# Kernel optimization log

Measured on AMD Instinct MI355X. Metric: run time of the kernel, lower is better.

The kernel has to match this reference:

```python
import jax, jax.numpy as jnp
import numpy as np

B, S, K, N = 4, 2048, 4096, 11008
GROUP_SIZE = 128
NUM_GROUPS = K // GROUP_SIZE  # 32


def setup_inputs() -> dict:
    key = jax.random.key(0)
    k1, k2, k3, k4, k5 = jax.random.split(key, 5)
    x = jax.random.normal(k1, (B, S, K), dtype=jnp.float32)
    # sensitivity-sorted column order is a permutation of [0, K)
    col_indices = jax.random.permutation(k2, K).astype(jnp.int32)
    # packed uint8 nibbles stored as int32 in [0, 256)
    w_packed = jax.random.randint(k3, (K // 2, N), 0, 256, dtype=jnp.int32)
    # per-group, per-output-column dequant scales (positive, small)
    scales = (jax.random.uniform(k4, (NUM_GROUPS, N), dtype=jnp.float32) + 0.05) * 0.01
    bias = jax.random.normal(k5, (N,), dtype=jnp.float32) * 0.01
    return {"x": x, "col_indices": col_indices, "w_packed": w_packed,
            "scales": scales, "bias": bias}


def _dequant_weight(w_packed, scales):
    # unpack int4 nibbles: low nibble -> even k, high nibble -> odd k
    low = (w_packed & 15) - 8          # [K//2, N]
    high = ((w_packed >> 4) & 15) - 8  # [K//2, N]
    w_int = jnp.stack([low, high], axis=1).reshape(K, N)  # interleaved [K, N]
    # per-group dequant: scale index = k // group_size
    w = w_int.astype(scales.dtype).reshape(NUM_GROUPS, GROUP_SIZE, N)
    w = w * scales[:, None, :]
    return w.reshape(K, N)


def reference(x, col_indices, w_packed, scales, bias):
    orig_shape = x.shape
    xm = x.reshape(-1, K)                     # [M, K]
    xg = jnp.take(xm, col_indices, axis=1)    # column-reorder gather [M, K]
    w = _dequant_weight(w_packed, scales)     # [K, N]
    out = jnp.einsum('mk,kn->mn', xg, w)      # fp32 accumulate
    out = out + bias
    return out.reshape(orig_shape[0], orig_shape[1], N)
```

## Files before the change

kernel.cpp:

```cpp
#include <hip/hip_runtime.h>
#include <hip/hip_bf16.h>
#include <stdint.h>

#define M_DIM 8192
#define K_DIM 4096
#define N_DIM 11008

typedef __attribute__((ext_vector_type(8))) short bf16x8;
typedef __attribute__((ext_vector_type(4))) float f32x4;
typedef __attribute__((ext_vector_type(16))) float f32x16;
typedef __attribute__((ext_vector_type(4))) unsigned int uint4v;

__device__ __forceinline__ unsigned short f2bf(float f) {
    __hip_bfloat16 h = __float2bfloat16(f);
    return __builtin_bit_cast(unsigned short, h);
}

__device__ __forceinline__ void gload_lds16(const unsigned short* g, unsigned short* l) {
    __builtin_amdgcn_global_load_lds(
        (const __attribute__((address_space(1))) void*)g,
        (__attribute__((address_space(3))) void*)l,
        16, 0, 0);
}

__device__ __forceinline__ unsigned lds_addr(const unsigned short* p) {
    return (unsigned)(uintptr_t)(const __attribute__((address_space(3))) unsigned short*)p;
}

#define DSRI(dst, a, OFF) asm volatile("ds_read_b128 %0, %1 offset:%2" \
    : "=v"(dst) : "v"(a), "n"(OFF) : "memory")

#define LGKM(N) do { \
    asm volatile("s_waitcnt lgkmcnt(" #N ")" ::: "memory"); \
    __builtin_amdgcn_sched_barrier(0); \
} while (0)
#define BAR() do { __builtin_amdgcn_s_barrier(); asm volatile("" ::: "memory"); } while (0)

__global__ void permute_x_kernel(const float* __restrict__ x,
                                 const int* __restrict__ ci,
                                 unsigned short* __restrict__ xg) {
    int idx = blockIdx.x * 256 + threadIdx.x;
    int64_t base = (int64_t)idx * 4;
    int m = (int)(base >> 12);
    int k = (int)(base & 4095);
    const float* xrow = x + ((int64_t)m << 12);
    int4 c4 = *reinterpret_cast<const int4*>(ci + k);
    ushort4 o;
    o.x = f2bf(xrow[c4.x]);
    o.y = f2bf(xrow[c4.y]);
    o.z = f2bf(xrow[c4.z]);
    o.w = f2bf(xrow[c4.w]);
    *reinterpret_cast<ushort4*>(xg + base) = o;
}

__global__ void dequant_w_kernel(const int* __restrict__ wp,
                                 const float* __restrict__ scales,
                                 unsigned short* __restrict__ wT) {
    __shared__ unsigned short tile[64][65];
    int n0 = blockIdx.x * 64;
    int k0 = blockIdx.y * 64;
    int g = k0 >> 7;
    int t = threadIdx.x;
    int col = t & 63;
    int r0 = t >> 6;
    float s = scales[(int64_t)g * N_DIM + n0 + col];
    int pr0 = k0 >> 1;
#pragma unroll
    for (int i = 0; i < 8; ++i) {
        int row = r0 + i * 4;
        int p = wp[(int64_t)(pr0 + row) * N_DIM + n0 + col];
        tile[2 * row][col]     = f2bf((float)((p & 15) - 8) * s);
        tile[2 * row + 1][col] = f2bf((float)(((p >> 4) & 15) - 8) * s);
    }
    __syncthreads();
    int nl = t >> 2;
    int kk0 = (t & 3) << 4;
    unsigned short vals[16];
#pragma unroll
    for (int j = 0; j < 16; ++j) vals[j] = tile[kk0 + j][nl];
    uint4v* dst = reinterpret_cast<uint4v*>(wT + (int64_t)(n0 + nl) * K_DIM + k0 + kk0);
    dst[0] = *reinterpret_cast<const uint4v*>(&vals[0]);
    dst[1] = *reinterpret_cast<const uint4v*>(&vals[8]);
}


__device__ __forceinline__ void mfma_tile(f32x16 (&acc)[4][2], const bf16x8 (&av)[4],
                                          const bf16x8 (&bv)[2]) {
    __builtin_amdgcn_s_setprio(1);
#pragma unroll
    for (int m = 0; m < 4; ++m)
#pragma unroll
        for (int n = 0; n < 2; ++n)
            acc[m][n] = __builtin_amdgcn_mfma_f32_32x32x16_bf16(
                av[m], bv[n], acc[m][n], 0, 0, 0);
    __builtin_amdgcn_s_setprio(0);
}

template <int BUF>
__device__ __forceinline__ void read_set(bf16x8 (&a)[4], bf16x8 (&b)[2],
                                         unsigned aB, unsigned aB2,
                                         unsigned bB, unsigned bB2) {
    const unsigned ad = (BUF < 2) ? aB : aB2;
    const unsigned bd = (BUF < 2) ? bB : bB2;
    constexpr int bo = (BUF < 2) ? BUF * 32768 : 0;
    DSRI(a[0], ad, bo + 0);
    DSRI(a[1], ad, bo + 2048);
    DSRI(a[2], ad, bo + 4096);
    DSRI(a[3], ad, bo + 6144);
    DSRI(b[0], bd, bo + 0);
    DSRI(b[1], bd, bo + 2048);
}

template <int DBUF, int ISB>
__device__ __forceinline__ void stage2(const unsigned short* p0, const unsigned short* p1,
                                       int t, unsigned short* lds, int wLds) {
    const unsigned short* s0 = p0 + t * 32;
    const unsigned short* s1 = p1 + t * 32;
    unsigned short* d = lds + DBUF * 16384 + ISB * 8192 + wLds;
    gload_lds16(s0, d);
    gload_lds16(s1, d + 512);
}

#define PH_TILE(B, BN, BS, CA_, CB_, NA_, NB_, tt)                        \
    do {                                                                  \
        read_set<B>(aZ, bZ, aK1, aK1_2, bK1, bK1_2);                      \
        stage2<BS, 0>(pA0, pA1, (tt), lds, wLds);                         \
        LGKM(6);                                                          \
        mfma_tile(acc, CA_, CB_);                                         \
        asm volatile("s_waitcnt vmcnt(2)" ::: "memory");                  \
        BAR();                                                            \
        read_set<BN>(NA_, NB_, aK0, aK0_2, bK0, bK0_2);                   \
        stage2<BS, 1>(pB0, pB1, (tt), lds, wLds);                         \
        LGKM(6);                                                          \
        mfma_tile(acc, aZ, bZ);                                           \
        BAR();                                                            \
    } while (0)

__global__ __launch_bounds__(512, 2)
void gemm_kernel(const unsigned short* __restrict__ A,
                 const unsigned short* __restrict__ BT,
                 const float* __restrict__ bias,
                 float* __restrict__ C) {
    __shared__ unsigned short lds[49152];

    constexpr int NT = N_DIM / 256;
    int wg = blockIdx.x, nwg = gridDim.x;
    int q = nwg >> 3, r = nwg & 7;
    int xcd = wg & 7, li = wg >> 3;
    int swz = (xcd < r ? xcd * (q + 1) : r * (q + 1) + (xcd - r) * q) + li;
    int by = swz / NT, bx = swz - by * NT;
    int brow = by << 8, bcol = bx << 8;

    int t = threadIdx.x;
    int lane = t & 63, w = t >> 6;
    int wr = w >> 2, wc = w & 3;
    int l31 = lane & 31, hi = lane >> 5;

    const unsigned xr = (unsigned)(((lane & 6) << 3) ^ ((lane & 16) << 1));
    const int riw = lane >> 2;
    const int s8 = ((lane & 3) ^ ((lane >> 3) & 3)) << 3;
    const int w32 = w * 32, wLds = w * 1024;

    const unsigned ldsB = lds_addr(lds);
    const unsigned lin_a = (unsigned)((wr * 128 + l31) * 64 + hi * 16);
    const unsigned lin_b = (unsigned)((wc * 64 + l31) * 64 + hi * 16);
    const unsigned aK0 = ldsB + (lin_a ^ xr);
    const unsigned aK1 = ldsB + ((lin_a + 32) ^ xr);
    const unsigned bK0 = ldsB + 16384u + (lin_b ^ xr);
    const unsigned bK1 = ldsB + 16384u + ((lin_b + 32) ^ xr);
    const unsigned aK0_2 = aK0 + 65536, aK1_2 = aK1 + 65536;
    const unsigned bK0_2 = bK0 + 65536, bK1_2 = bK1 + 65536;

    const unsigned short* pA0 = A + (int64_t)(brow + w32 + riw) * K_DIM + s8;
    const unsigned short* pA1 = A + (int64_t)(brow + w32 + 16 + riw) * K_DIM + (s8 ^ 16);
    const unsigned short* pB0 = BT + (int64_t)(bcol + w32 + riw) * K_DIM + s8;
    const unsigned short* pB1 = BT + (int64_t)(bcol + w32 + 16 + riw) * K_DIM + (s8 ^ 16);

    f32x16 acc[4][2];
#pragma unroll
    for (int m = 0; m < 4; ++m)
#pragma unroll
        for (int n = 0; n < 2; ++n)
#pragma unroll
            for (int j = 0; j < 16; ++j) acc[m][n][j] = 0.f;

    bf16x8 aX[4], bX[2], aY[4], bY[2], aZ[4], bZ[2];

    stage2<0, 0>(pA0, pA1, 0, lds, wLds);
    stage2<0, 1>(pB0, pB1, 0, lds, wLds);
    stage2<1, 0>(pA0, pA1, 1, lds, wLds);
    stage2<1, 1>(pB0, pB1, 1, lds, wLds);
    asm volatile("s_waitcnt vmcnt(4)" ::: "memory");
    BAR();
    read_set<0>(aX, bX, aK0, aK0_2, bK0, bK0_2);

#pragma unroll 1
    for (int body = 0; body < 21; ++body) {
        const int t2 = body * 6 + 2;
        PH_TILE(0, 1, 2, aX, bX, aY, bY, t2);
        PH_TILE(1, 2, 0, aY, bY, aX, bX, t2 + 1);
        PH_TILE(2, 0, 1, aX, bX, aY, bY, t2 + 2);
        PH_TILE(0, 1, 2, aY, bY, aX, bX, t2 + 3);
        PH_TILE(1, 2, 0, aX, bX, aY, bY, t2 + 4);
        PH_TILE(2, 0, 1, aY, bY, aX, bX, t2 + 5);
    }

    read_set<0>(aZ, bZ, aK1, aK1_2, bK1, bK1_2);
    LGKM(6);
    mfma_tile(acc, aX, bX);
    asm volatile("s_waitcnt vmcnt(0)" ::: "memory");
    BAR();
    read_set<1>(aY, bY, aK0, aK0_2, bK0, bK0_2);
    LGKM(6);
    mfma_tile(acc, aZ, bZ);
    BAR();
    read_set<1>(aZ, bZ, aK1, aK1_2, bK1, bK1_2);
    LGKM(6);
    mfma_tile(acc, aY, bY);
    LGKM(0);
    mfma_tile(acc, aZ, bZ);

    int orow0 = brow + wr * 128 + 4 * hi;
    int ocol0 = bcol + wc * 64 + l31;
#pragma unroll
    for (int n = 0; n < 2; ++n) {
        int col = ocol0 + n * 32;
        float bval = bias[col];
#pragma unroll
        for (int m = 0; m < 4; ++m) {
            int rbase = orow0 + m * 32;
#pragma unroll
            for (int j = 0; j < 16; ++j) {
                int row = rbase + (j & 3) + 8 * (j >> 2);
                C[(int64_t)row * N_DIM + col] = acc[m][n][j] + bval;
            }
        }
    }
}

extern "C" void kernel_launch(void* const* d_in, const int* in_sizes, int n_in,
                              void* d_out, int out_size, void* d_ws, size_t ws_size,
                              hipStream_t stream) {
    const float* x      = (const float*)d_in[0];
    const int* ci       = (const int*)d_in[1];
    const int* wp       = (const int*)d_in[2];
    const float* scales = (const float*)d_in[3];
    const float* bias   = (const float*)d_in[4];
    float* out          = (float*)d_out;

    const size_t wT_bytes = (size_t)N_DIM * K_DIM * 2;
    unsigned short* wT = (unsigned short*)d_ws;
    unsigned short* xg = wT + (size_t)N_DIM * K_DIM;

    size_t cap = (ws_size > wT_bytes) ? (ws_size - wT_bytes) : 0;
    int max_rows = (int)(cap / ((size_t)K_DIM * 2));
    int chunk_rows = (max_rows / 256) * 256;
    if (chunk_rows <= 0) chunk_rows = 256;
    if (chunk_rows > M_DIM) chunk_rows = M_DIM;

    dequant_w_kernel<<<dim3(N_DIM / 64, K_DIM / 64), 256, 0, stream>>>(wp, scales, wT);

    for (int m0 = 0; m0 < M_DIM; m0 += chunk_rows) {
        int rows = M_DIM - m0 < chunk_rows ? M_DIM - m0 : chunk_rows;
        int pgrid = (int)(((int64_t)rows * K_DIM) / (4 * 256));
        permute_x_kernel<<<pgrid, 256, 0, stream>>>(
            x + (int64_t)m0 * K_DIM, ci, xg);
        int grid = (rows / 256) * (N_DIM / 256);
        gemm_kernel<<<grid, 512, 0, stream>>>(
            xg, wT, bias, out + (int64_t)m0 * N_DIM);
    }
}
```

Before: 832.3 us.

## Shrink GEMM block tile to 128x256 with three-stage LDS ring and new swizzle

Halves the M extent of each workgroup tile, so each wave computes a 64x64 sub-tile. LDS becomes a three-buffer ring of combined A/B stages with a new XOR swizzle, and the per-k-step schedule issues loads before a single barrier. Launch bounds ask for higher occupancy and the grid doubles, aiming for better latency hiding and CU balance. In exchange, arithmetic intensity drops and B tile traffic from L2 doubles.

```diff
diff --git a/kernel.cpp b/kernel.cpp
--- a/kernel.cpp
+++ b/kernel.cpp
@@ -5,9 +5,9 @@
 #define M_DIM 8192
 #define K_DIM 4096
 #define N_DIM 11008
+#define NKT   (K_DIM / 32)
 
 typedef __attribute__((ext_vector_type(8))) short bf16x8;
-typedef __attribute__((ext_vector_type(4))) float f32x4;
 typedef __attribute__((ext_vector_type(16))) float f32x16;
 typedef __attribute__((ext_vector_type(4))) unsigned int uint4v;
 
@@ -84,11 +84,11 @@
 }
 
 
-__device__ __forceinline__ void mfma_tile(f32x16 (&acc)[4][2], const bf16x8 (&av)[4],
-                                          const bf16x8 (&bv)[2]) {
+__device__ __forceinline__ void mfma4(f32x16 (&acc)[2][2], const bf16x8 (&av)[2],
+                                      const bf16x8 (&bv)[2]) {
     __builtin_amdgcn_s_setprio(1);
 #pragma unroll
-    for (int m = 0; m < 4; ++m)
+    for (int m = 0; m < 2; ++m)
 #pragma unroll
         for (int n = 0; n < 2; ++n)
             acc[m][n] = __builtin_amdgcn_mfma_f32_32x32x16_bf16(
@@ -97,51 +97,43 @@
 }
 
 template <int BUF>
-__device__ __forceinline__ void read_set(bf16x8 (&a)[4], bf16x8 (&b)[2],
-                                         unsigned aB, unsigned aB2,
-                                         unsigned bB, unsigned bB2) {
-    const unsigned ad = (BUF < 2) ? aB : aB2;
-    const unsigned bd = (BUF < 2) ? bB : bB2;
-    constexpr int bo = (BUF < 2) ? BUF * 32768 : 0;
-    DSRI(a[0], ad, bo + 0);
-    DSRI(a[1], ad, bo + 2048);
-    DSRI(a[2], ad, bo + 4096);
-    DSRI(a[3], ad, bo + 6144);
-    DSRI(b[0], bd, bo + 0);
-    DSRI(b[1], bd, bo + 2048);
-}
-
-template <int DBUF, int ISB>
-__device__ __forceinline__ void stage2(const unsigned short* p0, const unsigned short* p1,
-                                       int t, unsigned short* lds, int wLds) {
-    const unsigned short* s0 = p0 + t * 32;
-    const unsigned short* s1 = p1 + t * 32;
-    unsigned short* d = lds + DBUF * 16384 + ISB * 8192 + wLds;
-    gload_lds16(s0, d);
-    gload_lds16(s1, d + 512);
+__device__ __forceinline__ void read_set(bf16x8 (&a)[2], bf16x8 (&b)[2],
+                                         unsigned aB, unsigned bB) {
+    DSRI(a[0], aB, BUF * 24576 + 0);
+    DSRI(a[1], aB, BUF * 24576 + 2048);
+    DSRI(b[0], bB, BUF * 24576 + 0);
+    DSRI(b[1], bB, BUF * 24576 + 2048);
+}
+
+template <int BS>
+__device__ __forceinline__ void stage3(const unsigned short* pA,
+                                       const unsigned short* pB,
+                                       int t, unsigned short* lds, int w) {
+    gload_lds16(pA + t * 32, lds + BS * 12288 + w * 512);
+    gload_lds16(pB + t * 32, lds + BS * 12288 + 4096 + w * 1024);
+    gload_lds16(pB + 16 * K_DIM + t * 32, lds + BS * 12288 + 4096 + w * 1024 + 512);
 }
 
 #define PH_TILE(B, BN, BS, CA_, CB_, NA_, NB_, tt)                        \
     do {                                                                  \
-        read_set<B>(aZ, bZ, aK1, aK1_2, bK1, bK1_2);                      \
-        stage2<BS, 0>(pA0, pA1, (tt), lds, wLds);                         \
-        LGKM(6);                                                          \
-        mfma_tile(acc, CA_, CB_);                                         \
-        asm volatile("s_waitcnt vmcnt(2)" ::: "memory");                  \
+        stage3<BS>(pA, pB, (tt), lds, w);                                 \
+        asm volatile("s_waitcnt vmcnt(3)" ::: "memory");                  \
         BAR();                                                            \
-        read_set<BN>(NA_, NB_, aK0, aK0_2, bK0, bK0_2);                   \
-        stage2<BS, 1>(pB0, pB1, (tt), lds, wLds);                         \
-        LGKM(6);                                                          \
-        mfma_tile(acc, aZ, bZ);                                           \
+        read_set<B>(aZ, bZ, aK1, bK1);                                    \
+        LGKM(4);                                                          \
+        mfma4(acc, CA_, CB_);                                             \
+        read_set<BN>(NA_, NB_, aK0, bK0);                                 \
+        LGKM(4);                                                          \
+        mfma4(acc, aZ, bZ);                                               \
         BAR();                                                            \
     } while (0)
 
-__global__ __launch_bounds__(512, 2)
+__global__ __launch_bounds__(512, 4)
 void gemm_kernel(const unsigned short* __restrict__ A,
                  const unsigned short* __restrict__ BT,
                  const float* __restrict__ bias,
                  float* __restrict__ C) {
-    __shared__ unsigned short lds[49152];
+    __shared__ unsigned short lds[36864];
 
     constexpr int NT = N_DIM / 256;
     int wg = blockIdx.x, nwg = gridDim.x;
@@ -149,50 +141,46 @@
     int xcd = wg & 7, li = wg >> 3;
     int swz = (xcd < r ? xcd * (q + 1) : r * (q + 1) + (xcd - r) * q) + li;
     int by = swz / NT, bx = swz - by * NT;
-    int brow = by << 8, bcol = bx << 8;
+    int brow = by << 7, bcol = bx << 8;
 
     int t = threadIdx.x;
     int lane = t & 63, w = t >> 6;
     int wr = w >> 2, wc = w & 3;
     int l31 = lane & 31, hi = lane >> 5;
 
-    const unsigned xr = (unsigned)(((lane & 6) << 3) ^ ((lane & 16) << 1));
+    const unsigned xr = (unsigned)(16 * ((l31 & 1) ^ ((l31 >> 2) & 1)) +
+                                   32 * ((l31 >> 1) & 1));
     const int riw = lane >> 2;
-    const int s8 = ((lane & 3) ^ ((lane >> 3) & 3)) << 3;
-    const int w32 = w * 32, wLds = w * 1024;
+    const int rr = riw & 7;
+    const int cperm = 8 * ((lane & 1) ^ (rr & 1) ^ ((rr >> 2) & 1)) +
+                      16 * (((lane >> 1) & 1) ^ ((rr >> 1) & 1));
 
     const unsigned ldsB = lds_addr(lds);
-    const unsigned lin_a = (unsigned)((wr * 128 + l31) * 64 + hi * 16);
+    const unsigned lin_a = (unsigned)((wr * 64 + l31) * 64 + hi * 16);
     const unsigned lin_b = (unsigned)((wc * 64 + l31) * 64 + hi * 16);
     const unsigned aK0 = ldsB + (lin_a ^ xr);
     const unsigned aK1 = ldsB + ((lin_a + 32) ^ xr);
-    const unsigned bK0 = ldsB + 16384u + (lin_b ^ xr);
-    const unsigned bK1 = ldsB + 16384u + ((lin_b + 32) ^ xr);
-    const unsigned aK0_2 = aK0 + 65536, aK1_2 = aK1 + 65536;
-    const unsigned bK0_2 = bK0 + 65536, bK1_2 = bK1 + 65536;
-
-    const unsigned short* pA0 = A + (int64_t)(brow + w32 + riw) * K_DIM + s8;
-    const unsigned short* pA1 = A + (int64_t)(brow + w32 + 16 + riw) * K_DIM + (s8 ^ 16);
-    const unsigned short* pB0 = BT + (int64_t)(bcol + w32 + riw) * K_DIM + s8;
-    const unsigned short* pB1 = BT + (int64_t)(bcol + w32 + 16 + riw) * K_DIM + (s8 ^ 16);
-
-    f32x16 acc[4][2];
-#pragma unroll
-    for (int m = 0; m < 4; ++m)
+    const unsigned bK0 = ldsB + 8192u + (lin_b ^ xr);
+    const unsigned bK1 = ldsB + 8192u + ((lin_b + 32) ^ xr);
+
+    const unsigned short* pA = A + (int64_t)(brow + w * 16 + riw) * K_DIM + cperm;
+    const unsigned short* pB = BT + (int64_t)(bcol + w * 32 + riw) * K_DIM + cperm;
+
+    f32x16 acc[2][2];
+#pragma unroll
+    for (int m = 0; m < 2; ++m)
 #pragma unroll
         for (int n = 0; n < 2; ++n)
 #pragma unroll
             for (int j = 0; j < 16; ++j) acc[m][n][j] = 0.f;
 
-    bf16x8 aX[4], bX[2], aY[4], bY[2], aZ[4], bZ[2];
-
-    stage2<0, 0>(pA0, pA1, 0, lds, wLds);
-    stage2<0, 1>(pB0, pB1, 0, lds, wLds);
-    stage2<1, 0>(pA0, pA1, 1, lds, wLds);
-    stage2<1, 1>(pB0, pB1, 1, lds, wLds);
-    asm volatile("s_waitcnt vmcnt(4)" ::: "memory");
+    bf16x8 aX[2], bX[2], aY[2], bY[2], aZ[2], bZ[2];
+
+    stage3<0>(pA, pB, 0, lds, w);
+    stage3<1>(pA, pB, 1, lds, w);
+    asm volatile("s_waitcnt vmcnt(3)" ::: "memory");
     BAR();
-    read_set<0>(aX, bX, aK0, aK0_2, bK0, bK0_2);
+    read_set<0>(aX, bX, aK0, bK0);
 
 #pragma unroll 1
     for (int body = 0; body < 21; ++body) {
@@ -205,29 +193,28 @@
         PH_TILE(2, 0, 1, aY, bY, aX, bX, t2 + 5);
     }
 
-    read_set<0>(aZ, bZ, aK1, aK1_2, bK1, bK1_2);
-    LGKM(6);
-    mfma_tile(acc, aX, bX);
     asm volatile("s_waitcnt vmcnt(0)" ::: "memory");
     BAR();
-    read_set<1>(aY, bY, aK0, aK0_2, bK0, bK0_2);
-    LGKM(6);
-    mfma_tile(acc, aZ, bZ);
-    BAR();
-    read_set<1>(aZ, bZ, aK1, aK1_2, bK1, bK1_2);
-    LGKM(6);
-    mfma_tile(acc, aY, bY);
+    read_set<0>(aZ, bZ, aK1, bK1);
+    LGKM(4);
+    mfma4(acc, aX, bX);
+    read_set<1>(aY, bY, aK0, bK0);
+    LGKM(4);
+    mfma4(acc, aZ, bZ);
+    read_set<1>(aZ, bZ, aK1, bK1);
+    LGKM(4);
+    mfma4(acc, aY, bY);
     LGKM(0);
-    mfma_tile(acc, aZ, bZ);
-
-    int orow0 = brow + wr * 128 + 4 * hi;
+    mfma4(acc, aZ, bZ);
+
+    int orow0 = brow + wr * 64 + 4 * hi;
     int ocol0 = bcol + wc * 64 + l31;
 #pragma unroll
     for (int n = 0; n < 2; ++n) {
         int col = ocol0 + n * 32;
         float bval = bias[col];
 #pragma unroll
-        for (int m = 0; m < 4; ++m) {
+        for (int m = 0; m < 2; ++m) {
             int rbase = orow0 + m * 32;
 #pragma unroll
             for (int j = 0; j < 16; ++j) {
@@ -254,8 +241,8 @@
 
     size_t cap = (ws_size > wT_bytes) ? (ws_size - wT_bytes) : 0;
     int max_rows = (int)(cap / ((size_t)K_DIM * 2));
-    int chunk_rows = (max_rows / 256) * 256;
-    if (chunk_rows <= 0) chunk_rows = 256;
+    int chunk_rows = (max_rows / 128) * 128;
+    if (chunk_rows <= 0) chunk_rows = 128;
     if (chunk_rows > M_DIM) chunk_rows = M_DIM;
 
     dequant_w_kernel<<<dim3(N_DIM / 64, K_DIM / 64), 256, 0, stream>>>(wp, scales, wT);
@@ -265,7 +252,7 @@
         int pgrid = (int)(((int64_t)rows * K_DIM) / (4 * 256));
         permute_x_kernel<<<pgrid, 256, 0, stream>>>(
             x + (int64_t)m0 * K_DIM, ci, xg);
-        int grid = (rows / 256) * (N_DIM / 256);
+        int grid = (rows / 128) * (N_DIM / 256);
         gemm_kernel<<<grid, 512, 0, stream>>>(
             xg, wT, bias, out + (int64_t)m0 * N_DIM);
     }
```

Measured after the change: 1.079 ms. +29.6%, slower.

## Restructure GEMM main loop to prefetch full next tile into registers

Applied to the files above, without the earlier changes.

Reworks the software pipeline so both K-halves of the next LDS tile are read into a second register set while the current tile's MFMAs run. One barrier per half-iteration now precedes reading the whole next tile, instead of interleaving half-tile reads around each MFMA group. This is meant to hide LDS read latency more fully behind MFMA work, at the cost of more VGPRs for the extra fragment buffers, which could hurt occupancy at launch bounds of 512 threads with 2 blocks per CU.

```diff
diff --git a/kernel.cpp b/kernel.cpp
--- a/kernel.cpp
+++ b/kernel.cpp
@@ -7,7 +7,6 @@
 #define N_DIM 11008
 
 typedef __attribute__((ext_vector_type(8))) short bf16x8;
-typedef __attribute__((ext_vector_type(4))) float f32x4;
 typedef __attribute__((ext_vector_type(16))) float f32x16;
 typedef __attribute__((ext_vector_type(4))) unsigned int uint4v;
 
@@ -121,18 +120,18 @@
     gload_lds16(s1, d + 512);
 }
 
-#define PH_TILE(B, BN, BS, CA_, CB_, NA_, NB_, tt)                        \
+#define PH_TILE(B, BN, BS, CA0, CB0, CA1, CB1, NA0, NB0, NA1, NB1, tt)    \
     do {                                                                  \
-        read_set<B>(aZ, bZ, aK1, aK1_2, bK1, bK1_2);                      \
         stage2<BS, 0>(pA0, pA1, (tt), lds, wLds);                         \
-        LGKM(6);                                                          \
-        mfma_tile(acc, CA_, CB_);                                         \
         asm volatile("s_waitcnt vmcnt(2)" ::: "memory");                  \
         BAR();                                                            \
-        read_set<BN>(NA_, NB_, aK0, aK0_2, bK0, bK0_2);                   \
+        read_set<BN>(NA0, NB0, aK0, aK0_2, bK0, bK0_2);                   \
+        LGKM(12);                                                         \
+        mfma_tile(acc, CA0, CB0);                                         \
         stage2<BS, 1>(pB0, pB1, (tt), lds, wLds);                         \
-        LGKM(6);                                                          \
-        mfma_tile(acc, aZ, bZ);                                           \
+        read_set<BN>(NA1, NB1, aK1, aK1_2, bK1, bK1_2);                   \
+        LGKM(12);                                                         \
+        mfma_tile(acc, CA1, CB1);                                         \
         BAR();                                                            \
     } while (0)
 
@@ -184,7 +183,8 @@
 #pragma unroll
             for (int j = 0; j < 16; ++j) acc[m][n][j] = 0.f;
 
-    bf16x8 aX[4], bX[2], aY[4], bY[2], aZ[4], bZ[2];
+    bf16x8 aE0[4], bE0[2], aE1[4], bE1[2];
+    bf16x8 aO0[4], bO0[2], aO1[4], bO1[2];
 
     stage2<0, 0>(pA0, pA1, 0, lds, wLds);
     stage2<0, 1>(pB0, pB1, 0, lds, wLds);
@@ -192,33 +192,32 @@
     stage2<1, 1>(pB0, pB1, 1, lds, wLds);
     asm volatile("s_waitcnt vmcnt(4)" ::: "memory");
     BAR();
-    read_set<0>(aX, bX, aK0, aK0_2, bK0, bK0_2);
+    read_set<0>(aE0, bE0, aK0, aK0_2, bK0, bK0_2);
+    read_set<0>(aE1, bE1, aK1, aK1_2, bK1, bK1_2);
 
 #pragma unroll 1
     for (int body = 0; body < 21; ++body) {
         const int t2 = body * 6 + 2;
-        PH_TILE(0, 1, 2, aX, bX, aY, bY, t2);
-        PH_TILE(1, 2, 0, aY, bY, aX, bX, t2 + 1);
-        PH_TILE(2, 0, 1, aX, bX, aY, bY, t2 + 2);
-        PH_TILE(0, 1, 2, aY, bY, aX, bX, t2 + 3);
-        PH_TILE(1, 2, 0, aX, bX, aY, bY, t2 + 4);
-        PH_TILE(2, 0, 1, aY, bY, aX, bX, t2 + 5);
-    }
-
-    read_set<0>(aZ, bZ, aK1, aK1_2, bK1, bK1_2);
-    LGKM(6);
-    mfma_tile(acc, aX, bX);
+        PH_TILE(0, 1, 2, aE0, bE0, aE1, bE1, aO0, bO0, aO1, bO1, t2);
+        PH_TILE(1, 2, 0, aO0, bO0, aO1, bO1, aE0, bE0, aE1, bE1, t2 + 1);
+        PH_TILE(2, 0, 1, aE0, bE0, aE1, bE1, aO0, bO0, aO1, bO1, t2 + 2);
+        PH_TILE(0, 1, 2, aO0, bO0, aO1, bO1, aE0, bE0, aE1, bE1, t2 + 3);
+        PH_TILE(1, 2, 0, aE0, bE0, aE1, bE1, aO0, bO0, aO1, bO1, t2 + 4);
+        PH_TILE(2, 0, 1, aO0, bO0, aO1, bO1, aE0, bE0, aE1, bE1, t2 + 5);
+    }
+
     asm volatile("s_waitcnt vmcnt(0)" ::: "memory");
     BAR();
-    read_set<1>(aY, bY, aK0, aK0_2, bK0, bK0_2);
+    read_set<1>(aO0, bO0, aK0, aK0_2, bK0, bK0_2);
+    LGKM(12);
+    mfma_tile(acc, aE0, bE0);
+    read_set<1>(aO1, bO1, aK1, aK1_2, bK1, bK1_2);
+    LGKM(12);
+    mfma_tile(acc, aE1, bE1);
     LGKM(6);
-    mfma_tile(acc, aZ, bZ);
-    BAR();
-    read_set<1>(aZ, bZ, aK1, aK1_2, bK1, bK1_2);
-    LGKM(6);
-    mfma_tile(acc, aY, bY);
+    mfma_tile(acc, aO0, bO0);
     LGKM(0);
-    mfma_tile(acc, aZ, bZ);
+    mfma_tile(acc, aO1, bO1);
 
     int orow0 = brow + wr * 128 + 4 * hi;
     int ocol0 = bcol + wc * 64 + l31;
```

Result: slower. 877.7 us (+5.5%).
